# Performance work log

Hardware: AMD Instinct MI355X
Metric: run time of the kernel (lower is better)

The kernel has to match this reference:

```python
import jax, jax.numpy as jnp
import numpy as np

T, N, R = 10, 50000, 50000   # time steps, nodes per graph, total restaurants
D_IN, D, H = 128, 64, 4      # input dim, hidden dim, attention heads
E = 400000                   # edges per timestep (before self-loops)
HD = D // H                  # head dim


def setup_inputs() -> dict:
    key = jax.random.key(0)
    ks = jax.random.split(key, 16)
    inp = {}
    inp["x"] = jax.random.normal(ks[0], (T, N, D_IN), jnp.float32)
    inp["edge_index"] = jax.random.randint(ks[1], (T, 2, E), 0, N, jnp.int32)
    inp["edge_weight"] = jax.random.uniform(ks[2], (T, E), jnp.float32)
    # per-timestep permutation mapping local node idx -> global restaurant idx
    inp["global_idx"] = jax.vmap(lambda k: jax.random.permutation(k, R))(
        jax.random.split(ks[3], T)).astype(jnp.int32)
    s = 0.05
    inp["gcn1_w"] = jax.random.normal(ks[4], (D, D_IN), jnp.float32) * s
    inp["gcn1_b"] = jnp.zeros((D,), jnp.float32)
    inp["gcn2_w"] = jax.random.normal(ks[5], (D, D), jnp.float32) * s
    inp["gcn2_b"] = jnp.zeros((D,), jnp.float32)
    inp["in_proj_w"] = jax.random.normal(ks[6], (3 * D, D), jnp.float32) * s
    inp["in_proj_b"] = jnp.zeros((3 * D,), jnp.float32)
    inp["out_proj_w"] = jax.random.normal(ks[7], (D, D), jnp.float32) * s
    inp["out_proj_b"] = jnp.zeros((D,), jnp.float32)
    inp["w1"] = jnp.ones((T, D), jnp.float32)
    inp["w2"] = jnp.ones((T, D), jnp.float32)
    inp["w3"] = jnp.ones((D,), jnp.float32)
    inp["w4"] = jnp.ones((D,), jnp.float32)
    inp["ln1_g"] = jnp.ones((D,), jnp.float32)
    inp["ln1_b"] = jnp.zeros((D,), jnp.float32)
    inp["ln2_g"] = jnp.ones((D,), jnp.float32)
    inp["ln2_b"] = jnp.zeros((D,), jnp.float32)
    inp["fc_w"] = jax.random.normal(ks[8], (D, D), jnp.float32) * s
    inp["fc_b"] = jnp.zeros((D,), jnp.float32)
    return inp


def _layer_norm(x, g, b, eps=1e-5):
    mu = jnp.mean(x, axis=-1, keepdims=True)
    var = jnp.mean((x - mu) ** 2, axis=-1, keepdims=True)
    return (x - mu) * jax.lax.rsqrt(var + eps) * g + b


def _gcn_layer(h, src, dst, ew, W, b):
    # PyG GCNConv with edge weights; self-loops already appended by caller.
    deg = jax.ops.segment_sum(ew, dst, num_segments=N)
    dinv = jnp.where(deg > 0, jax.lax.rsqrt(deg), 0.0)
    norm = dinv[src] * ew * dinv[dst]                      # [E+N]
    hw = h @ W.T                                           # [N, D]
    agg = jax.ops.segment_sum(norm[:, None] * hw[src], dst, num_segments=N)
    return agg + b


def _forward(x, edge_index, edge_weight, global_idx,
             gcn1_w, gcn1_b, gcn2_w, gcn2_b,
             in_proj_w, in_proj_b, out_proj_w, out_proj_b,
             w1, w2, w3, w4, ln1_g, ln1_b, ln2_g, ln2_b, fc_w, fc_b):
    loop = jnp.arange(N, dtype=edge_index.dtype)
    src = jnp.concatenate([edge_index[:, 0], jnp.broadcast_to(loop, (T, N))], axis=1)
    dst = jnp.concatenate([edge_index[:, 1], jnp.broadcast_to(loop, (T, N))], axis=1)
    ew = jnp.concatenate([edge_weight, jnp.ones((T, N), edge_weight.dtype)], axis=1)

    def per_t(xt, st, dt, wt):
        h = jax.nn.relu(_gcn_layer(xt, st, dt, wt, gcn1_w, gcn1_b))
        return jax.nn.relu(_gcn_layer(h, st, dt, wt, gcn2_w, gcn2_b))

    feat = jax.vmap(per_t)(x, src, dst, ew)                # [T, N, D]

    # scatter local features to global alignment (permutation per timestep)
    aligned = jax.vmap(lambda g, f: jnp.zeros((R, D), f.dtype).at[g].set(f))(
        global_idx, feat)                                  # [T, R, D]
    time_embeds = jnp.transpose(aligned, (1, 0, 2))        # [R, T, D]

    presence = jax.vmap(
        lambda g: jnp.zeros((R,), bool).at[g].set(True))(global_idx)  # [T, R]
    key_padding_mask = ~presence.T                          # [R, T], True = ignore
    bias = jnp.where(key_padding_mask, -1e9, 0.0)           # [R, T]

    # multi-head self-attention over time axis (batch_first, batch = R)
    qkv = time_embeds @ in_proj_w.T + in_proj_b             # [R, T, 3D]
    q, k, v = jnp.split(qkv, 3, axis=-1)
    q = q.reshape(R, T, H, HD)
    k = k.reshape(R, T, H, HD)
    v = v.reshape(R, T, H, HD)
    scores = jnp.einsum('rthd,rshd->rhts', q, k) / np.sqrt(HD)
    scores = scores + bias[:, None, None, :]
    attn = jax.nn.softmax(scores, axis=-1)                  # [R, H, T, T]
    ao = jnp.einsum('rhts,rshd->rthd', attn, v).reshape(R, T, D)
    attn_out = ao @ out_proj_w.T + out_proj_b               # [R, T, D]

    # dropouts are identity in eval mode
    time_feat = _layer_norm(w1 * time_embeds + w2 * attn_out, ln1_g, ln1_b)
    final = time_feat[:, -1, :]                             # [R, D]
    out = final @ fc_w.T + fc_b                             # [R, D]
    return _layer_norm(w3 * final + w4 * out, ln2_g, ln2_b)


def reference(x, edge_index, edge_weight, global_idx,
              gcn1_w, gcn1_b, gcn2_w, gcn2_b,
              in_proj_w, in_proj_b, out_proj_w, out_proj_b,
              w1, w2, w3, w4, ln1_g, ln1_b, ln2_g, ln2_b, fc_w, fc_b):
    return _forward(x, edge_index, edge_weight, global_idx,
                    gcn1_w, gcn1_b, gcn2_w, gcn2_b,
                    in_proj_w, in_proj_b, out_proj_w, out_proj_b,
                    w1, w2, w3, w4, ln1_g, ln1_b, ln2_g, ln2_b, fc_w, fc_b)
```

## Files before the change

### kernel.cpp

```cpp
#include <hip/hip_runtime.h>
#include <cstdint>
#include <cstddef>

namespace {

constexpr int T = 10;
constexpr int N = 50000;
constexpr int R = 50000;
constexpr int DIN = 128;
constexpr int D = 64;
constexpr int E = 400000;

constexpr int BINS = 16384;
constexpr int NR = 4;
constexpr int SEG = 25;
constexpr int ESEG = E / SEG;
constexpr int EV4 = ESEG / 4;

constexpr float WSCALE = 262144.0f;
constexpr float WINV = 1.0f / 262144.0f;

typedef _Float16 h16;
typedef __attribute__((ext_vector_type(8))) _Float16 f16x8;
typedef __attribute__((ext_vector_type(4))) _Float16 f16x4;
typedef __attribute__((ext_vector_type(4))) float f32x4;

__global__ __launch_bounds__(256) void k_hist(const int* __restrict__ ei,
                                              const float* __restrict__ ew,
                                              unsigned* __restrict__ pu) {
  __shared__ unsigned h[BINS];
  int b = blockIdx.x;
  int s = b % SEG;
  int tr = b / SEG;
  int r = tr % NR;
  int t = tr / NR;
  for (int i = threadIdx.x; i < BINS; i += 256) h[i] = 0u;
  __syncthreads();
  int bin0 = r * BINS;
  const int4* dst4 = (const int4*)(ei + (size_t)t * 2 * E + E + s * ESEG);
  const float4* ew4 = (const float4*)(ew + (size_t)t * E + s * ESEG);
  for (int i = threadIdx.x; i < EV4; i += 256) {
    int4 d = dst4[i];
    float4 w = ew4[i];
    unsigned a0 = (unsigned)(d.x - bin0);
    unsigned a1 = (unsigned)(d.y - bin0);
    unsigned a2 = (unsigned)(d.z - bin0);
    unsigned a3 = (unsigned)(d.w - bin0);
    if (a0 < (unsigned)BINS) atomicAdd(&h[a0], 0x1000000u + (unsigned)fmaf(w.x, WSCALE, 0.5f));
    if (a1 < (unsigned)BINS) atomicAdd(&h[a1], 0x1000000u + (unsigned)fmaf(w.y, WSCALE, 0.5f));
    if (a2 < (unsigned)BINS) atomicAdd(&h[a2], 0x1000000u + (unsigned)fmaf(w.z, WSCALE, 0.5f));
    if (a3 < (unsigned)BINS) atomicAdd(&h[a3], 0x1000000u + (unsigned)fmaf(w.w, WSCALE, 0.5f));
  }
  __syncthreads();
  size_t base = (size_t)b * BINS;
  for (int i = threadIdx.x; i < BINS; i += 256) pu[base + i] = h[i];
}

__global__ __launch_bounds__(256) void k_hreduce2(unsigned* __restrict__ pu,
                                                  int* __restrict__ cnt,
                                                  float* __restrict__ dinv,
                                                  int* __restrict__ rowptr,
                                                  int* __restrict__ tbase) {
  int t = blockIdx.y;
  int n = blockIdx.x * 256 + threadIdx.x;
  int lane = threadIdx.x & 63, wid = threadIdx.x >> 6;
  __shared__ int wsum[4];
  __shared__ int base_s;
  unsigned cs[SEG];
  unsigned c = 0, wacc = 0;
  bool ok = (n < N);
  int r = 0, rel = 0;
  if (ok) {
    r = n / BINS; rel = n - r * BINS;
    #pragma unroll
    for (int s = 0; s < SEG; ++s) {
      unsigned v = pu[((size_t)((t * NR + r) * SEG + s)) * BINS + rel];
      cs[s] = v >> 24;
      c += cs[s];
      wacc += v & 0xFFFFFFu;
    }
    cnt[t * N + n] = (int)c;
    dinv[t * N + n] = rsqrtf(1.0f + (float)wacc * WINV);
  }
  int sv = (int)c;
  #pragma unroll
  for (int off = 1; off < 64; off <<= 1) {
    int u = __shfl_up(sv, off, 64);
    if (lane >= off) sv += u;
  }
  if (lane == 63) wsum[wid] = sv;
  __syncthreads();
  int wadd = 0;
  #pragma unroll
  for (int w = 0; w < 4; ++w) if (w < wid) wadd += wsum[w];
  if (threadIdx.x == 255) base_s = atomicAdd(&tbase[t], wadd + sv);
  __syncthreads();
  if (ok) {
    unsigned run = (unsigned)(base_s + wadd + sv - (int)c);
    rowptr[t * N + n] = (int)run;
    #pragma unroll
    for (int s = 0; s < SEG; ++s) {
      size_t b = ((size_t)((t * NR + r) * SEG + s)) * BINS + rel;
      pu[b] = run;
      run += cs[s];
    }
  }
}

__global__ __launch_bounds__(256) void k_fill2(const int* __restrict__ ei,
                                               const float* __restrict__ ew,
                                               const unsigned* __restrict__ pu,
                                               int2* __restrict__ pk) {
  __shared__ int cur[BINS];
  int b = blockIdx.x;
  int s = b % SEG;
  int tr = b / SEG;
  int r = tr % NR;
  int t = tr / NR;
  size_t pbase = (size_t)b * BINS;
  for (int i = threadIdx.x; i < BINS; i += 256) cur[i] = (int)pu[pbase + i];
  __syncthreads();
  int bin0 = r * BINS;
  const int4* src4 = (const int4*)(ei + (size_t)t * 2 * E + s * ESEG);
  const int4* dst4 = (const int4*)(ei + (size_t)t * 2 * E + E + s * ESEG);
  const float4* ew4 = (const float4*)(ew + (size_t)t * E + s * ESEG);
  int2* pkt = pk + (size_t)t * E;
  for (int i = threadIdx.x; i < EV4; i += 256) {
    int4 d = dst4[i];
    int4 sv = src4[i];
    float4 w = ew4[i];
    unsigned a0 = (unsigned)(d.x - bin0);
    unsigned a1 = (unsigned)(d.y - bin0);
    unsigned a2 = (unsigned)(d.z - bin0);
    unsigned a3 = (unsigned)(d.w - bin0);
    if (a0 < (unsigned)BINS) {
      int pos = atomicAdd(&cur[a0], 1);
      pkt[pos] = make_int2(sv.x, __float_as_int(w.x));
    }
    if (a1 < (unsigned)BINS) {
      int pos = atomicAdd(&cur[a1], 1);
      pkt[pos] = make_int2(sv.y, __float_as_int(w.y));
    }
    if (a2 < (unsigned)BINS) {
      int pos = atomicAdd(&cur[a2], 1);
      pkt[pos] = make_int2(sv.z, __float_as_int(w.z));
    }
    if (a3 < (unsigned)BINS) {
      int pos = atomicAdd(&cur[a3], 1);
      pkt[pos] = make_int2(sv.w, __float_as_int(w.w));
    }
  }
}

__global__ __launch_bounds__(256) void k_prep(const float* __restrict__ g1w,
                                              const float* __restrict__ g2w,
                                              const float* __restrict__ inw,
                                              const float* __restrict__ outw,
                                              const float* __restrict__ fcw,
                                              h16* __restrict__ Wb,
                                              int* __restrict__ tbase) {
  int i = blockIdx.x * 256 + threadIdx.x;
  if (i >= 32768) {
    if (i < 32768 + 16) tbase[i - 32768] = 0;
    return;
  }
  const float* src;
  int off;
  if (i < 8192)       { src = g1w;  off = 0; }
  else if (i < 12288) { src = g2w;  off = 8192; }
  else if (i < 24576) { src = inw;  off = 12288; }
  else if (i < 28672) { src = outw; off = 24576; }
  else                { src = fcw;  off = 28672; }
  Wb[i] = (h16)src[i - off];
}

template <int K, int NT, bool F16B, int MODE>
__global__ __launch_bounds__(256) void k_mm(const h16* __restrict__ Wb,
                                            const void* __restrict__ Bv,
                                            const float* __restrict__ biasp,
                                            h16* __restrict__ out,
                                            int Mwaves) {
  int wv = threadIdx.x >> 6, lane = threadIdx.x & 63;
  int wave = blockIdx.x * 4 + wv;
  if (wave >= Mwaves) return;
  int m0 = wave * 16;
  int half = lane & 15, quad = lane >> 4;
  constexpr int KS = K / 32;
  int m = m0 + half;
  float ds = 1.0f;
  if (MODE == 2) ds = biasp[m];
  f16x8 bfrag[KS];
  if (F16B) {
    const h16* Bp = (const h16*)Bv + (size_t)m * K + quad * 8;
    #pragma unroll
    for (int ks = 0; ks < KS; ++ks) bfrag[ks] = *(const f16x8*)(Bp + ks * 32);
  } else {
    const float* Bp = (const float*)Bv + (size_t)m * K + quad * 8;
    #pragma unroll
    for (int ks = 0; ks < KS; ++ks) {
      float4 f0 = *(const float4*)(Bp + ks * 32);
      float4 f1 = *(const float4*)(Bp + ks * 32 + 4);
      f16x8 b;
      b[0] = (h16)f0.x; b[1] = (h16)f0.y; b[2] = (h16)f0.z; b[3] = (h16)f0.w;
      b[4] = (h16)f1.x; b[5] = (h16)f1.y; b[6] = (h16)f1.z; b[7] = (h16)f1.w;
      bfrag[ks] = b;
    }
  }
  #pragma unroll
  for (int jt = 0; jt < NT; ++jt) {
    f32x4 acc = {0.f, 0.f, 0.f, 0.f};
    const h16* Wp = Wb + (size_t)(jt * 16 + half) * K + quad * 8;
    #pragma unroll
    for (int ks = 0; ks < KS; ++ks) {
      f16x8 afrag = *(const f16x8*)(Wp + ks * 32);
      acc = __builtin_amdgcn_mfma_f32_16x16x32_f16(afrag, bfrag[ks], acc, 0, 0, 0);
    }
    int j = jt * 16 + quad * 4;
    if (MODE == 2) {
      acc[0] *= ds; acc[1] *= ds; acc[2] *= ds; acc[3] *= ds;
    }
    f16x4 o;
    o[0] = (h16)acc[0]; o[1] = (h16)acc[1]; o[2] = (h16)acc[2]; o[3] = (h16)acc[3];
    *(f16x4*)(out + (size_t)m * (NT * 16) + j) = o;
  }
}

template <bool SCATTER>
__global__ __launch_bounds__(256) void k_gather(
    const h16* __restrict__ hw, const int2* __restrict__ pk,
    const float* __restrict__ dinv, const int* __restrict__ rowptr,
    const int* __restrict__ cnt, const float* __restrict__ bias,
    const int* __restrict__ gidx, h16* __restrict__ outp) {
  __shared__ __align__(16) float red[4][8][68];
  int wv = threadIdx.x >> 6, lane = threadIdx.x & 63;
  int t = blockIdx.y;
  int nd = lane >> 5;
  int grp = (lane >> 3) & 3;
  int sub = lane & 7;
  int n = blockIdx.x * 8 + wv * 2 + nd;
  const h16* hwt = hw + (size_t)t * N * D;
  const int2* pkt = pk + (size_t)t * E;
  int start = rowptr[t * N + n];
  int m = cnt[t * N + n];
  int nA = blockIdx.x * 8 + wv * 2;
  int nB = nA + 1;
  float selfA = (float)hwt[(size_t)nA * D + lane];
  float selfB = (float)hwt[(size_t)nB * D + lane];
  float dnA = dinv[t * N + nA];
  float dnB = dinv[t * N + nB];
  float bi = bias[lane];
  f32x4 accL = {0.f, 0.f, 0.f, 0.f};
  f32x4 accH = {0.f, 0.f, 0.f, 0.f};
  int e = grp;
  for (; e + 12 < m; e += 16) {
    int2 r0 = pkt[start + e];
    int2 r1 = pkt[start + e + 4];
    int2 r2 = pkt[start + e + 8];
    int2 r3 = pkt[start + e + 12];
    float w0 = __int_as_float(r0.y);
    float w1 = __int_as_float(r1.y);
    float w2 = __int_as_float(r2.y);
    float w3 = __int_as_float(r3.y);
    f16x8 h0 = *(const f16x8*)(hwt + (size_t)r0.x * D + sub * 8);
    f16x8 h1 = *(const f16x8*)(hwt + (size_t)r1.x * D + sub * 8);
    f16x8 h2 = *(const f16x8*)(hwt + (size_t)r2.x * D + sub * 8);
    f16x8 h3 = *(const f16x8*)(hwt + (size_t)r3.x * D + sub * 8);
    #pragma unroll
    for (int j = 0; j < 4; ++j) {
      accL[j] = fmaf(w0, (float)h0[j], accL[j]);
      accH[j] = fmaf(w0, (float)h0[j + 4], accH[j]);
    }
    #pragma unroll
    for (int j = 0; j < 4; ++j) {
      accL[j] = fmaf(w1, (float)h1[j], accL[j]);
      accH[j] = fmaf(w1, (float)h1[j + 4], accH[j]);
    }
    #pragma unroll
    for (int j = 0; j < 4; ++j) {
      accL[j] = fmaf(w2, (float)h2[j], accL[j]);
      accH[j] = fmaf(w2, (float)h2[j + 4], accH[j]);
    }
    #pragma unroll
    for (int j = 0; j < 4; ++j) {
      accL[j] = fmaf(w3, (float)h3[j], accL[j]);
      accH[j] = fmaf(w3, (float)h3[j + 4], accH[j]);
    }
  }
  for (; e + 4 < m; e += 8) {
    int2 ra = pkt[start + e];
    int2 rb = pkt[start + e + 4];
    float wa = __int_as_float(ra.y);
    float wb = __int_as_float(rb.y);
    f16x8 ha = *(const f16x8*)(hwt + (size_t)ra.x * D + sub * 8);
    f16x8 hb = *(const f16x8*)(hwt + (size_t)rb.x * D + sub * 8);
    #pragma unroll
    for (int j = 0; j < 4; ++j) {
      accL[j] = fmaf(wa, (float)ha[j], accL[j]);
      accH[j] = fmaf(wa, (float)ha[j + 4], accH[j]);
    }
    #pragma unroll
    for (int j = 0; j < 4; ++j) {
      accL[j] = fmaf(wb, (float)hb[j], accL[j]);
      accH[j] = fmaf(wb, (float)hb[j + 4], accH[j]);
    }
  }
  if (e < m) {
    int2 ra = pkt[start + e];
    float wa = __int_as_float(ra.y);
    f16x8 ha = *(const f16x8*)(hwt + (size_t)ra.x * D + sub * 8);
    #pragma unroll
    for (int j = 0; j < 4; ++j) {
      accL[j] = fmaf(wa, (float)ha[j], accL[j]);
      accH[j] = fmaf(wa, (float)ha[j + 4], accH[j]);
    }
  }
  float* rw = &red[wv][nd * 4 + grp][sub * 8];
  *(f32x4*)(rw) = accL;
  *(f32x4*)(rw + 4) = accH;
  __builtin_amdgcn_wave_barrier();
  #pragma unroll
  for (int d2 = 0; d2 < 2; ++d2) {
    int nn = nA + d2;
    float s = red[wv][d2 * 4 + 0][lane] + red[wv][d2 * 4 + 1][lane] +
              red[wv][d2 * 4 + 2][lane] + red[wv][d2 * 4 + 3][lane];
    float selfv = d2 ? selfB : selfA;
    float dn = d2 ? dnB : dnA;
    float v = fmaxf(fmaf(dn, s + selfv, bi), 0.f);
    size_t ro;
    if (SCATTER) {
      int rr2 = gidx[(size_t)t * R + nn];
      ro = ((size_t)rr2 * T + t) * D + lane;
    } else {
      ro = ((size_t)t * N + nn) * D + lane;
    }
    outp[ro] = (h16)v;
  }
}

constexpr int KVP = 132;
constexpr int P72 = 72;

__global__ __launch_bounds__(256) void k_tail(
    const h16* __restrict__ te,
    const h16* __restrict__ WIb,
    const float* __restrict__ inB,
    const h16* __restrict__ WOb,
    const float* __restrict__ outB,
    const h16* __restrict__ WFb,
    const float* __restrict__ fcB,
    const float* __restrict__ w1,
    const float* __restrict__ w2,
    const float* __restrict__ w3,
    const float* __restrict__ w4,
    const float* __restrict__ g1, const float* __restrict__ b1,
    const float* __restrict__ g2, const float* __restrict__ b2,
    float* __restrict__ outp) {
  __shared__ __align__(16) h16 kvl[160][KVP];
  __shared__ __align__(16) h16 ql[16][P72];
  __shared__ __align__(16) h16 aol[16][P72];
  __shared__ __align__(16) h16 tbuf[16][P72];
  __shared__ __align__(16) h16 fbuf[16][P72];
  __shared__ __align__(16) float pf[16][64];

  int wv = threadIdx.x >> 6, lane = threadIdx.x & 63;
  int half = lane & 15, quad = lane >> 4;
  int g0 = blockIdx.x * 160;

  for (int tt = wv; tt < 10; tt += 4) {
    int lr = tt * 16 + half;
    const h16* Bp = te + (size_t)(g0 + lr) * 64 + quad * 8;
    f16x8 b0 = *(const f16x8*)(Bp);
    f16x8 b1f = *(const f16x8*)(Bp + 32);
    int rloc = lr / 10;
    bool isq = (lr - rloc * 10) == 9;
    #pragma unroll
    for (int jt = 0; jt < 12; ++jt) {
      f32x4 acc = {0.f, 0.f, 0.f, 0.f};
      const h16* Wp = WIb + (size_t)(jt * 16 + half) * 64 + quad * 8;
      acc = __builtin_amdgcn_mfma_f32_16x16x32_f16(*(const f16x8*)(Wp), b0, acc, 0, 0, 0);
      acc = __builtin_amdgcn_mfma_f32_16x16x32_f16(*(const f16x8*)(Wp + 32), b1f, acc, 0, 0, 0);
      int j = jt * 16 + quad * 4;
      float4 b4 = *(const float4*)(inB + j);
      f16x4 o;
      o[0] = (h16)(acc[0] + b4.x); o[1] = (h16)(acc[1] + b4.y);
      o[2] = (h16)(acc[2] + b4.z); o[3] = (h16)(acc[3] + b4.w);
      if (jt < 4) {
        if (isq) *(f16x4*)(&ql[rloc][j]) = o;
      } else {
        *(f16x4*)(&kvl[lr][j - 64]) = o;
      }
    }
  }
  __syncthreads();

  #pragma unroll
  for (int i = 0; i < 4; ++i) {
    int rl = wv * 4 + i;
    float qv = (float)ql[rl][lane];
    float sc[T], vv[T];
    #pragma unroll
    for (int s = 0; s < T; ++s) {
      float kk = (float)kvl[rl * 10 + s][lane];
      vv[s] = (float)kvl[rl * 10 + s][64 + lane];
      float p = qv * kk;
      p += __shfl_xor(p, 8, 16);
      p += __shfl_xor(p, 4, 16);
      p += __shfl_xor(p, 2, 16);
      p += __shfl_xor(p, 1, 16);
      sc[s] = p * 0.25f;
    }
    float mx = sc[0];
    #pragma unroll
    for (int s = 1; s < T; ++s) mx = fmaxf(mx, sc[s]);
    float ssum = 0.f;
    #pragma unroll
    for (int s = 0; s < T; ++s) { sc[s] = expf(sc[s] - mx); ssum += sc[s]; }
    float rinv = 1.0f / ssum;
    float aov = 0.f;
    #pragma unroll
    for (int s = 0; s < T; ++s) aov = fmaf(sc[s] * rinv, vv[s], aov);
    aol[rl][lane] = (h16)aov;
  }
  __syncthreads();

  {
    const h16* Bp = &aol[half][quad * 8];
    f16x8 b0 = *(const f16x8*)(Bp);
    f16x8 b1f = *(const f16x8*)(Bp + 32);
    f32x4 acc = {0.f, 0.f, 0.f, 0.f};
    const h16* Wp = WOb + (size_t)(wv * 16 + half) * 64 + quad * 8;
    acc = __builtin_amdgcn_mfma_f32_16x16x32_f16(*(const f16x8*)(Wp), b0, acc, 0, 0, 0);
    acc = __builtin_amdgcn_mfma_f32_16x16x32_f16(*(const f16x8*)(Wp + 32), b1f, acc, 0, 0, 0);
    int j = wv * 16 + quad * 4;
    float4 b4 = *(const float4*)(outB + j);
    f16x4 o;
    o[0] = (h16)(acc[0] + b4.x); o[1] = (h16)(acc[1] + b4.y);
    o[2] = (h16)(acc[2] + b4.z); o[3] = (h16)(acc[3] + b4.w);
    *(f16x4*)(&tbuf[half][j]) = o;
  }
  __syncthreads();

  {
    float w1l = w1[(T - 1) * 64 + lane];
    float w2l = w2[(T - 1) * 64 + lane];
    float g1l = g1[lane], b1l = b1[lane];
    #pragma unroll
    for (int i = 0; i < 4; ++i) {
      int rl = wv * 4 + i;
      float t9 = (float)te[(size_t)(g0 + rl * 10 + 9) * 64 + lane];
      float pr = (float)tbuf[rl][lane];
      float pre = w1l * t9 + w2l * pr;
      float s1 = pre;
      #pragma unroll
      for (int off = 32; off >= 1; off >>= 1) s1 += __shfl_xor(s1, off, 64);
      float mu = s1 * (1.0f / 64.0f);
      float dv = pre - mu;
      float s2 = dv * dv;
      #pragma unroll
      for (int off = 32; off >= 1; off >>= 1) s2 += __shfl_xor(s2, off, 64);
      float rstd = 1.0f / sqrtf(s2 * (1.0f / 64.0f) + 1e-5f);
      float fin = dv * rstd * g1l + b1l;
      pf[rl][lane] = fin;
      fbuf[rl][lane] = (h16)fin;
    }
  }
  __syncthreads();

  {
    const h16* Bp = &fbuf[half][quad * 8];
    f16x8 b0 = *(const f16x8*)(Bp);
    f16x8 b1f = *(const f16x8*)(Bp + 32);
    f32x4 acc = {0.f, 0.f, 0.f, 0.f};
    const h16* Wp = WFb + (size_t)(wv * 16 + half) * 64 + quad * 8;
    acc = __builtin_amdgcn_mfma_f32_16x16x32_f16(*(const f16x8*)(Wp), b0, acc, 0, 0, 0);
    acc = __builtin_amdgcn_mfma_f32_16x16x32_f16(*(const f16x8*)(Wp + 32), b1f, acc, 0, 0, 0);
    int j = wv * 16 + quad * 4;
    float4 b4 = *(const float4*)(fcB + j);
    f16x4 o;
    o[0] = (h16)(acc[0] + b4.x); o[1] = (h16)(acc[1] + b4.y);
    o[2] = (h16)(acc[2] + b4.z); o[3] = (h16)(acc[3] + b4.w);
    *(f16x4*)(&tbuf[half][j]) = o;
  }
  __syncthreads();

  {
    float w3l = w3[lane], w4l = w4[lane];
    float g2l = g2[lane], b2l = b2[lane];
    #pragma unroll
    for (int i = 0; i < 4; ++i) {
      int rl = wv * 4 + i;
      float fin = pf[rl][lane];
      float oo = (float)tbuf[rl][lane];
      float pre = w3l * fin + w4l * oo;
      float s1 = pre;
      #pragma unroll
      for (int off = 32; off >= 1; off >>= 1) s1 += __shfl_xor(s1, off, 64);
      float mu = s1 * (1.0f / 64.0f);
      float dv = pre - mu;
      float s2 = dv * dv;
      #pragma unroll
      for (int off = 32; off >= 1; off >>= 1) s2 += __shfl_xor(s2, off, 64);
      float rstd = 1.0f / sqrtf(s2 * (1.0f / 64.0f) + 1e-5f);
      outp[(size_t)(blockIdx.x * 16 + rl) * 64 + lane] = dv * rstd * g2l + b2l;
    }
  }
}

}

extern "C" void kernel_launch(void* const* d_in, const int* in_sizes, int n_in,
                              void* d_out, int out_size, void* d_ws, size_t ws_size,
                              hipStream_t stream) {
  const float* x      = (const float*)d_in[0];
  const int*   ei     = (const int*)d_in[1];
  const float* ew     = (const float*)d_in[2];
  const int*   gidx   = (const int*)d_in[3];
  const float* gcn1_w = (const float*)d_in[4];
  const float* gcn1_b = (const float*)d_in[5];
  const float* gcn2_w = (const float*)d_in[6];
  const float* gcn2_b = (const float*)d_in[7];
  const float* in_w   = (const float*)d_in[8];
  const float* in_b   = (const float*)d_in[9];
  const float* out_w  = (const float*)d_in[10];
  const float* out_b  = (const float*)d_in[11];
  const float* w1     = (const float*)d_in[12];
  const float* w2     = (const float*)d_in[13];
  const float* w3     = (const float*)d_in[14];
  const float* w4     = (const float*)d_in[15];
  const float* ln1_g  = (const float*)d_in[16];
  const float* ln1_b  = (const float*)d_in[17];
  const float* ln2_g  = (const float*)d_in[18];
  const float* ln2_b  = (const float*)d_in[19];
  const float* fc_w   = (const float*)d_in[20];
  const float* fc_b   = (const float*)d_in[21];
  float* outp = (float*)d_out;

  char* ws = (char*)d_ws;
  size_t off = 0;
  auto alloc = [&](size_t bytes) {
    void* p = ws + off;
    off += (bytes + 255) & ~(size_t)255;
    return p;
  };
  h16* h1te = (h16*)alloc(sizeof(h16) * (size_t)T * N * D);
  h16* Wb   = (h16*)alloc(sizeof(h16) * 32768);
  int* tbase = (int*)alloc(sizeof(int) * 16);
  float* dinv   = (float*)alloc(sizeof(float) * T * N);
  int*   cnt    = (int*)alloc(sizeof(int) * T * N);
  int*   rowptr = (int*)alloc(sizeof(int) * T * N);
  int2*  pk     = (int2*)alloc(sizeof(int2) * (size_t)T * E);
  size_t pu_off = off;
  unsigned* pu  = (unsigned*)alloc(sizeof(unsigned) * (size_t)T * NR * SEG * BINS);
  h16* hw = (h16*)(ws + pu_off);
  size_t hw_end = pu_off + sizeof(h16) * (size_t)T * N * D;
  if (hw_end > off) off = hw_end;

  const h16* W1b = Wb;
  const h16* W2b = Wb + 8192;
  const h16* WIb = Wb + 12288;
  const h16* WOb = Wb + 24576;
  const h16* WFb = Wb + 28672;

  const int M = T * N;
  const int MW = M / 16;
  const int PREP_BLOCKS = T * NR * SEG;

  k_prep<<<129, 256, 0, stream>>>(gcn1_w, gcn2_w, in_w, out_w, fc_w, Wb, tbase);

  k_hist<<<PREP_BLOCKS, 256, 0, stream>>>(ei, ew, pu);
  dim3 hg((N + 255) / 256, T);
  k_hreduce2<<<hg, 256, 0, stream>>>(pu, cnt, dinv, rowptr, tbase);
  k_fill2<<<PREP_BLOCKS, 256, 0, stream>>>(ei, ew, pu, pk);

  dim3 gg(N / 8, T);
  k_mm<DIN, 4, false, 2><<<(MW + 3) / 4, 256, 0, stream>>>(W1b, x, dinv, hw, MW);
  k_gather<false><<<gg, 256, 0, stream>>>(hw, pk, dinv, rowptr, cnt, gcn1_b, nullptr, h1te);
  k_mm<D, 4, true, 2><<<(MW + 3) / 4, 256, 0, stream>>>(W2b, h1te, dinv, hw, MW);
  k_gather<true><<<gg, 256, 0, stream>>>(hw, pk, dinv, rowptr, cnt, gcn2_b, gidx, h1te);

  k_tail<<<R / 16, 256, 0, stream>>>(h1te, WIb, in_b, WOb, out_b, WFb, fc_b,
                                     w1, w2, w3, w4, ln1_g, ln1_b, ln2_g, ln2_b, outp);
}
```

Before: 978.0 us.

## Replace LDS-binned CSR build with global atomics and pack edges into 32 bits

The segmented shared-memory histogram and fill, where every block rescanned all edges for its bin range, are replaced by single-pass kernels that use global atomics on per-node counters. The reduce kernel now reads one counter per node instead of 25 partials, and zeroing of the counter array is folded into the prep kernel. Edge records shrink from int2 to one 32-bit word (16-bit source index plus fp16 weight), cutting the traffic of the CSR write and the gather reads. The risks are global-atomic contention, lower weight precision, and source indices above 65535 being truncated (N=50000 fits).

```diff
diff --git a/kernel.cpp b/kernel.cpp
--- a/kernel.cpp
+++ b/kernel.cpp
@@ -10,12 +10,7 @@
 constexpr int DIN = 128;
 constexpr int D = 64;
 constexpr int E = 400000;
-
-constexpr int BINS = 16384;
-constexpr int NR = 4;
-constexpr int SEG = 25;
-constexpr int ESEG = E / SEG;
-constexpr int EV4 = ESEG / 4;
+constexpr int EV4 = E / 4;
 
 constexpr float WSCALE = 262144.0f;
 constexpr float WINV = 1.0f / 262144.0f;
@@ -25,131 +20,17 @@
 typedef __attribute__((ext_vector_type(4))) _Float16 f16x4;
 typedef __attribute__((ext_vector_type(4))) float f32x4;
 
-__global__ __launch_bounds__(256) void k_hist(const int* __restrict__ ei,
-                                              const float* __restrict__ ew,
-                                              unsigned* __restrict__ pu) {
-  __shared__ unsigned h[BINS];
-  int b = blockIdx.x;
-  int s = b % SEG;
-  int tr = b / SEG;
-  int r = tr % NR;
-  int t = tr / NR;
-  for (int i = threadIdx.x; i < BINS; i += 256) h[i] = 0u;
-  __syncthreads();
-  int bin0 = r * BINS;
-  const int4* dst4 = (const int4*)(ei + (size_t)t * 2 * E + E + s * ESEG);
-  const float4* ew4 = (const float4*)(ew + (size_t)t * E + s * ESEG);
-  for (int i = threadIdx.x; i < EV4; i += 256) {
-    int4 d = dst4[i];
-    float4 w = ew4[i];
-    unsigned a0 = (unsigned)(d.x - bin0);
-    unsigned a1 = (unsigned)(d.y - bin0);
-    unsigned a2 = (unsigned)(d.z - bin0);
-    unsigned a3 = (unsigned)(d.w - bin0);
-    if (a0 < (unsigned)BINS) atomicAdd(&h[a0], 0x1000000u + (unsigned)fmaf(w.x, WSCALE, 0.5f));
-    if (a1 < (unsigned)BINS) atomicAdd(&h[a1], 0x1000000u + (unsigned)fmaf(w.y, WSCALE, 0.5f));
-    if (a2 < (unsigned)BINS) atomicAdd(&h[a2], 0x1000000u + (unsigned)fmaf(w.z, WSCALE, 0.5f));
-    if (a3 < (unsigned)BINS) atomicAdd(&h[a3], 0x1000000u + (unsigned)fmaf(w.w, WSCALE, 0.5f));
-  }
-  __syncthreads();
-  size_t base = (size_t)b * BINS;
-  for (int i = threadIdx.x; i < BINS; i += 256) pu[base + i] = h[i];
-}
-
-__global__ __launch_bounds__(256) void k_hreduce2(unsigned* __restrict__ pu,
-                                                  int* __restrict__ cnt,
-                                                  float* __restrict__ dinv,
-                                                  int* __restrict__ rowptr,
-                                                  int* __restrict__ tbase) {
-  int t = blockIdx.y;
-  int n = blockIdx.x * 256 + threadIdx.x;
-  int lane = threadIdx.x & 63, wid = threadIdx.x >> 6;
-  __shared__ int wsum[4];
-  __shared__ int base_s;
-  unsigned cs[SEG];
-  unsigned c = 0, wacc = 0;
-  bool ok = (n < N);
-  int r = 0, rel = 0;
-  if (ok) {
-    r = n / BINS; rel = n - r * BINS;
-    #pragma unroll
-    for (int s = 0; s < SEG; ++s) {
-      unsigned v = pu[((size_t)((t * NR + r) * SEG + s)) * BINS + rel];
-      cs[s] = v >> 24;
-      c += cs[s];
-      wacc += v & 0xFFFFFFu;
-    }
-    cnt[t * N + n] = (int)c;
-    dinv[t * N + n] = rsqrtf(1.0f + (float)wacc * WINV);
-  }
-  int sv = (int)c;
-  #pragma unroll
-  for (int off = 1; off < 64; off <<= 1) {
-    int u = __shfl_up(sv, off, 64);
-    if (lane >= off) sv += u;
-  }
-  if (lane == 63) wsum[wid] = sv;
-  __syncthreads();
-  int wadd = 0;
-  #pragma unroll
-  for (int w = 0; w < 4; ++w) if (w < wid) wadd += wsum[w];
-  if (threadIdx.x == 255) base_s = atomicAdd(&tbase[t], wadd + sv);
-  __syncthreads();
-  if (ok) {
-    unsigned run = (unsigned)(base_s + wadd + sv - (int)c);
-    rowptr[t * N + n] = (int)run;
-    #pragma unroll
-    for (int s = 0; s < SEG; ++s) {
-      size_t b = ((size_t)((t * NR + r) * SEG + s)) * BINS + rel;
-      pu[b] = run;
-      run += cs[s];
-    }
-  }
-}
-
-__global__ __launch_bounds__(256) void k_fill2(const int* __restrict__ ei,
-                                               const float* __restrict__ ew,
-                                               const unsigned* __restrict__ pu,
-                                               int2* __restrict__ pk) {
-  __shared__ int cur[BINS];
-  int b = blockIdx.x;
-  int s = b % SEG;
-  int tr = b / SEG;
-  int r = tr % NR;
-  int t = tr / NR;
-  size_t pbase = (size_t)b * BINS;
-  for (int i = threadIdx.x; i < BINS; i += 256) cur[i] = (int)pu[pbase + i];
-  __syncthreads();
-  int bin0 = r * BINS;
-  const int4* src4 = (const int4*)(ei + (size_t)t * 2 * E + s * ESEG);
-  const int4* dst4 = (const int4*)(ei + (size_t)t * 2 * E + E + s * ESEG);
-  const float4* ew4 = (const float4*)(ew + (size_t)t * E + s * ESEG);
-  int2* pkt = pk + (size_t)t * E;
-  for (int i = threadIdx.x; i < EV4; i += 256) {
-    int4 d = dst4[i];
-    int4 sv = src4[i];
-    float4 w = ew4[i];
-    unsigned a0 = (unsigned)(d.x - bin0);
-    unsigned a1 = (unsigned)(d.y - bin0);
-    unsigned a2 = (unsigned)(d.z - bin0);
-    unsigned a3 = (unsigned)(d.w - bin0);
-    if (a0 < (unsigned)BINS) {
-      int pos = atomicAdd(&cur[a0], 1);
-      pkt[pos] = make_int2(sv.x, __float_as_int(w.x));
-    }
-    if (a1 < (unsigned)BINS) {
-      int pos = atomicAdd(&cur[a1], 1);
-      pkt[pos] = make_int2(sv.y, __float_as_int(w.y));
-    }
-    if (a2 < (unsigned)BINS) {
-      int pos = atomicAdd(&cur[a2], 1);
-      pkt[pos] = make_int2(sv.z, __float_as_int(w.z));
-    }
-    if (a3 < (unsigned)BINS) {
-      int pos = atomicAdd(&cur[a3], 1);
-      pkt[pos] = make_int2(sv.w, __float_as_int(w.w));
-    }
-  }
+__device__ __forceinline__ unsigned short f16bits(float f) {
+  _Float16 h = (_Float16)f;
+  unsigned short b;
+  __builtin_memcpy(&b, &h, 2);
+  return b;
+}
+__device__ __forceinline__ float upw(unsigned r) {
+  unsigned short b = (unsigned short)(r & 0xFFFFu);
+  _Float16 h;
+  __builtin_memcpy(&h, &b, 2);
+  return (float)h;
 }
 
 __global__ __launch_bounds__(256) void k_prep(const float* __restrict__ g1w,
@@ -158,20 +39,101 @@
                                               const float* __restrict__ outw,
                                               const float* __restrict__ fcw,
                                               h16* __restrict__ Wb,
+                                              unsigned* __restrict__ pu32,
                                               int* __restrict__ tbase) {
   int i = blockIdx.x * 256 + threadIdx.x;
-  if (i >= 32768) {
-    if (i < 32768 + 16) tbase[i - 32768] = 0;
-    return;
-  }
-  const float* src;
-  int off;
-  if (i < 8192)       { src = g1w;  off = 0; }
-  else if (i < 12288) { src = g2w;  off = 8192; }
-  else if (i < 24576) { src = inw;  off = 12288; }
-  else if (i < 28672) { src = outw; off = 24576; }
-  else                { src = fcw;  off = 28672; }
-  Wb[i] = (h16)src[i - off];
+  if (i < 32768) {
+    const float* src;
+    int off;
+    if (i < 8192)       { src = g1w;  off = 0; }
+    else if (i < 12288) { src = g2w;  off = 8192; }
+    else if (i < 24576) { src = inw;  off = 12288; }
+    else if (i < 28672) { src = outw; off = 24576; }
+    else                { src = fcw;  off = 28672; }
+    Wb[i] = (h16)src[i - off];
+  }
+  if (i < 16) tbase[i] = 0;
+  if (i < T * N) pu32[i] = 0u;
+}
+
+__global__ __launch_bounds__(256) void k_count(const int* __restrict__ ei,
+                                               const float* __restrict__ ew,
+                                               unsigned* __restrict__ pu32) {
+  int t = blockIdx.y;
+  int i = blockIdx.x * 256 + threadIdx.x;
+  if (i >= EV4) return;
+  const int4* dst4 = (const int4*)(ei + (size_t)t * 2 * E + E);
+  const float4* ew4 = (const float4*)(ew + (size_t)t * E);
+  int4 d = dst4[i];
+  float4 w = ew4[i];
+  unsigned* put = pu32 + (size_t)t * N;
+  atomicAdd(&put[d.x], 0x1000000u + (unsigned)fmaf(w.x, WSCALE, 0.5f));
+  atomicAdd(&put[d.y], 0x1000000u + (unsigned)fmaf(w.y, WSCALE, 0.5f));
+  atomicAdd(&put[d.z], 0x1000000u + (unsigned)fmaf(w.z, WSCALE, 0.5f));
+  atomicAdd(&put[d.w], 0x1000000u + (unsigned)fmaf(w.w, WSCALE, 0.5f));
+}
+
+__global__ __launch_bounds__(256) void k_hred3(const unsigned* __restrict__ pu32,
+                                               int* __restrict__ cnt,
+                                               float* __restrict__ dinv,
+                                               int* __restrict__ rowptr,
+                                               unsigned* __restrict__ cur,
+                                               int* __restrict__ tbase) {
+  int t = blockIdx.y;
+  int n = blockIdx.x * 256 + threadIdx.x;
+  int lane = threadIdx.x & 63, wid = threadIdx.x >> 6;
+  __shared__ int wsum[4];
+  __shared__ int base_s;
+  bool ok = (n < N);
+  unsigned v = ok ? pu32[(size_t)t * N + n] : 0u;
+  unsigned c = v >> 24;
+  if (ok) {
+    cnt[t * N + n] = (int)c;
+    dinv[t * N + n] = rsqrtf(1.0f + (float)(v & 0xFFFFFFu) * WINV);
+  }
+  int sv = (int)c;
+  #pragma unroll
+  for (int off = 1; off < 64; off <<= 1) {
+    int u = __shfl_up(sv, off, 64);
+    if (lane >= off) sv += u;
+  }
+  if (lane == 63) wsum[wid] = sv;
+  __syncthreads();
+  int wadd = 0;
+  #pragma unroll
+  for (int w = 0; w < 4; ++w) if (w < wid) wadd += wsum[w];
+  if (threadIdx.x == 255) base_s = atomicAdd(&tbase[t], wadd + sv);
+  __syncthreads();
+  if (ok) {
+    int run = base_s + wadd + sv - (int)c;
+    rowptr[t * N + n] = run;
+    cur[t * N + n] = (unsigned)run;
+  }
+}
+
+__global__ __launch_bounds__(256) void k_fill3(const int* __restrict__ ei,
+                                               const float* __restrict__ ew,
+                                               unsigned* __restrict__ cur,
+                                               unsigned* __restrict__ pk) {
+  int t = blockIdx.y;
+  int i = blockIdx.x * 256 + threadIdx.x;
+  if (i >= EV4) return;
+  const int4* src4 = (const int4*)(ei + (size_t)t * 2 * E);
+  const int4* dst4 = (const int4*)(ei + (size_t)t * 2 * E + E);
+  const float4* ew4 = (const float4*)(ew + (size_t)t * E);
+  int4 sv = src4[i];
+  int4 d = dst4[i];
+  float4 w = ew4[i];
+  unsigned* curt = cur + (size_t)t * N;
+  unsigned* pkt = pk + (size_t)t * E;
+  unsigned p0 = atomicAdd(&curt[d.x], 1u);
+  pkt[p0] = ((unsigned)sv.x << 16) | f16bits(w.x);
+  unsigned p1 = atomicAdd(&curt[d.y], 1u);
+  pkt[p1] = ((unsigned)sv.y << 16) | f16bits(w.y);
+  unsigned p2 = atomicAdd(&curt[d.z], 1u);
+  pkt[p2] = ((unsigned)sv.z << 16) | f16bits(w.z);
+  unsigned p3 = atomicAdd(&curt[d.w], 1u);
+  pkt[p3] = ((unsigned)sv.w << 16) | f16bits(w.w);
 }
 
 template <int K, int NT, bool F16B, int MODE>
@@ -227,7 +189,7 @@
 
 template <bool SCATTER>
 __global__ __launch_bounds__(256) void k_gather(
-    const h16* __restrict__ hw, const int2* __restrict__ pk,
+    const h16* __restrict__ hw, const unsigned* __restrict__ pk,
     const float* __restrict__ dinv, const int* __restrict__ rowptr,
     const int* __restrict__ cnt, const float* __restrict__ bias,
     const int* __restrict__ gidx, h16* __restrict__ outp) {
@@ -239,7 +201,7 @@
   int sub = lane & 7;
   int n = blockIdx.x * 8 + wv * 2 + nd;
   const h16* hwt = hw + (size_t)t * N * D;
-  const int2* pkt = pk + (size_t)t * E;
+  const unsigned* pkt = pk + (size_t)t * E;
   int start = rowptr[t * N + n];
   int m = cnt[t * N + n];
   int nA = blockIdx.x * 8 + wv * 2;
@@ -253,18 +215,18 @@
   f32x4 accH = {0.f, 0.f, 0.f, 0.f};
   int e = grp;
   for (; e + 12 < m; e += 16) {
-    int2 r0 = pkt[start + e];
-    int2 r1 = pkt[start + e + 4];
-    int2 r2 = pkt[start + e + 8];
-    int2 r3 = pkt[start + e + 12];
-    float w0 = __int_as_float(r0.y);
-    float w1 = __int_as_float(r1.y);
-    float w2 = __int_as_float(r2.y);
-    float w3 = __int_as_float(r3.y);
-    f16x8 h0 = *(const f16x8*)(hwt + (size_t)r0.x * D + sub * 8);
-    f16x8 h1 = *(const f16x8*)(hwt + (size_t)r1.x * D + sub * 8);
-    f16x8 h2 = *(const f16x8*)(hwt + (size_t)r2.x * D + sub * 8);
-    f16x8 h3 = *(const f16x8*)(hwt + (size_t)r3.x * D + sub * 8);
+    unsigned r0 = pkt[start + e];
+    unsigned r1 = pkt[start + e + 4];
+    unsigned r2 = pkt[start + e + 8];
+    unsigned r3 = pkt[start + e + 12];
+    float w0 = upw(r0);
+    float w1 = upw(r1);
+    float w2 = upw(r2);
+    float w3 = upw(r3);
+    f16x8 h0 = *(const f16x8*)(hwt + (size_t)(r0 >> 16) * D + sub * 8);
+    f16x8 h1 = *(const f16x8*)(hwt + (size_t)(r1 >> 16) * D + sub * 8);
+    f16x8 h2 = *(const f16x8*)(hwt + (size_t)(r2 >> 16) * D + sub * 8);
+    f16x8 h3 = *(const f16x8*)(hwt + (size_t)(r3 >> 16) * D + sub * 8);
     #pragma unroll
     for (int j = 0; j < 4; ++j) {
       accL[j] = fmaf(w0, (float)h0[j], accL[j]);
@@ -287,12 +249,12 @@
     }
   }
   for (; e + 4 < m; e += 8) {
-    int2 ra = pkt[start + e];
-    int2 rb = pkt[start + e + 4];
-    float wa = __int_as_float(ra.y);
-    float wb = __int_as_float(rb.y);
-    f16x8 ha = *(const f16x8*)(hwt + (size_t)ra.x * D + sub * 8);
-    f16x8 hb = *(const f16x8*)(hwt + (size_t)rb.x * D + sub * 8);
+    unsigned ra = pkt[start + e];
+    unsigned rb = pkt[start + e + 4];
+    float wa = upw(ra);
+    float wb = upw(rb);
+    f16x8 ha = *(const f16x8*)(hwt + (size_t)(ra >> 16) * D + sub * 8);
+    f16x8 hb = *(const f16x8*)(hwt + (size_t)(rb >> 16) * D + sub * 8);
     #pragma unroll
     for (int j = 0; j < 4; ++j) {
       accL[j] = fmaf(wa, (float)ha[j], accL[j]);
@@ -305,9 +267,9 @@
     }
   }
   if (e < m) {
-    int2 ra = pkt[start + e];
-    float wa = __int_as_float(ra.y);
-    f16x8 ha = *(const f16x8*)(hwt + (size_t)ra.x * D + sub * 8);
+    unsigned ra = pkt[start + e];
+    float wa = upw(ra);
+    f16x8 ha = *(const f16x8*)(hwt + (size_t)(ra >> 16) * D + sub * 8);
     #pragma unroll
     for (int j = 0; j < 4; ++j) {
       accL[j] = fmaf(wa, (float)ha[j], accL[j]);
@@ -548,11 +510,12 @@
   float* dinv   = (float*)alloc(sizeof(float) * T * N);
   int*   cnt    = (int*)alloc(sizeof(int) * T * N);
   int*   rowptr = (int*)alloc(sizeof(int) * T * N);
-  int2*  pk     = (int2*)alloc(sizeof(int2) * (size_t)T * E);
-  size_t pu_off = off;
-  unsigned* pu  = (unsigned*)alloc(sizeof(unsigned) * (size_t)T * NR * SEG * BINS);
-  h16* hw = (h16*)(ws + pu_off);
-  size_t hw_end = pu_off + sizeof(h16) * (size_t)T * N * D;
+  unsigned* pk  = (unsigned*)alloc(sizeof(unsigned) * (size_t)T * E);
+  size_t u_base = off;
+  unsigned* pu32 = (unsigned*)alloc(sizeof(unsigned) * T * N);
+  unsigned* cur  = (unsigned*)alloc(sizeof(unsigned) * T * N);
+  h16* hw = (h16*)(ws + u_base);
+  size_t hw_end = u_base + sizeof(h16) * (size_t)T * N * D;
   if (hw_end > off) off = hw_end;
 
   const h16* W1b = Wb;
@@ -563,14 +526,15 @@
 
   const int M = T * N;
   const int MW = M / 16;
-  const int PREP_BLOCKS = T * NR * SEG;
-
-  k_prep<<<129, 256, 0, stream>>>(gcn1_w, gcn2_w, in_w, out_w, fc_w, Wb, tbase);
-
-  k_hist<<<PREP_BLOCKS, 256, 0, stream>>>(ei, ew, pu);
+
+  k_prep<<<(T * N + 255) / 256, 256, 0, stream>>>(gcn1_w, gcn2_w, in_w, out_w, fc_w,
+                                                  Wb, pu32, tbase);
+
+  dim3 eg((EV4 + 255) / 256, T);
+  k_count<<<eg, 256, 0, stream>>>(ei, ew, pu32);
   dim3 hg((N + 255) / 256, T);
-  k_hreduce2<<<hg, 256, 0, stream>>>(pu, cnt, dinv, rowptr, tbase);
-  k_fill2<<<PREP_BLOCKS, 256, 0, stream>>>(ei, ew, pu, pk);
+  k_hred3<<<hg, 256, 0, stream>>>(pu32, cnt, dinv, rowptr, cur, tbase);
+  k_fill3<<<eg, 256, 0, stream>>>(ei, ew, cur, pk);
 
   dim3 gg(N / 8, T);
   k_mm<DIN, 4, false, 2><<<(MW + 3) / 4, 256, 0, stream>>>(W1b, x, dinv, hw, MW);
```

New measurement: 1.252 ms. 28.1% more time.
